# Optimization experiments

Hardware: AMD Instinct MI355X
Metric: run time of the kernel (lower is better)

Reference implementation:

```python
import jax, jax.numpy as jnp
import numpy as np

B, P = 256, 4096
H, W = 512, 512


def setup_inputs() -> dict:
    key = jax.random.key(0)
    k1, k2, k3 = jax.random.split(key, 3)
    indices = jax.random.randint(k1, (B, P, 2), 0, min(H, W), dtype=jnp.int64)
    num_valid = jax.random.randint(k2, (B,), 0, P, dtype=jnp.int32)
    feats = jax.random.normal(k3, (B, P, 1), dtype=jnp.float32)
    return {"indices": indices, "num_valid_coordinates": num_valid, "padded_features": feats}


def reference(indices, num_valid_coordinates, padded_features):
    # mask of valid (non-padded) points per sample: [B, P]
    mask = jnp.arange(P, dtype=num_valid_coordinates.dtype)[None, :] < num_valid_coordinates[:, None]
    vals = jnp.squeeze(padded_features, axis=-1) * mask.astype(padded_features.dtype)  # [B, P]
    # send invalid points out of bounds so JAX drops those scatter writes
    idx = jnp.where(mask[:, :, None], indices, H)  # [B, P, 2]
    b = jnp.broadcast_to(jnp.arange(B)[:, None], (B, P))
    out = jnp.zeros((B, H, W), dtype=padded_features.dtype)
    # single vectorized batched scatter-add (duplicate coordinates sum,
    # matching SparseTensor densification semantics)
    out = out.at[b, idx[..., 0], idx[..., 1]].add(vals)
    return out
```

## Files before the change

kernel.cpp:

```cpp
#include <hip/hip_runtime.h>

#define BATCH 256
#define PTS   4096
#define HH    512
#define WW    512

#define ROWS_PER_TILE 16
#define TILES (HH / ROWS_PER_TILE)
#define TILE_ELEMS (ROWS_PER_TILE * WW)

typedef float f32x4 __attribute__((ext_vector_type(4)));

__global__ __launch_bounds__(256) void tile_gather_kernel(
        const int* __restrict__ indices,
        const int* __restrict__ num_valid,
        const float* __restrict__ feats,
        float* __restrict__ out)
{
    __shared__ float tile[TILE_ELEMS];

    int i = blockIdx.x;
    int xcd  = i & 7;
    int slot = i >> 3;
    int b = xcd * (BATCH / 8) + (slot >> 5);
    int t = slot & (TILES - 1);
    int r0 = t * ROWS_PER_TILE;
    int tidx = threadIdx.x;

    f32x4* tile4 = reinterpret_cast<f32x4*>(tile);
    #pragma unroll
    for (int k = tidx; k < TILE_ELEMS / 4; k += 256)
        tile4[k] = (f32x4){0.f, 0.f, 0.f, 0.f};

    int nv = num_valid[b];
    __syncthreads();

    const int4* idx4 = reinterpret_cast<const int4*>(indices) + (size_t)b * (PTS / 2);
    const float* fb  = feats + (size_t)b * PTS;

    int n4 = (nv + 1) >> 1;
    for (int q = tidx; q < n4; q += 256) {
        int4 two = idx4[q];
        int r0a = two.x - r0;
        if ((unsigned)r0a < ROWS_PER_TILE)
            atomicAdd(&tile[r0a * WW + two.y], fb[2 * q]);
        int p1 = 2 * q + 1;
        int r1a = two.z - r0;
        if (p1 < nv && (unsigned)r1a < ROWS_PER_TILE)
            atomicAdd(&tile[r1a * WW + two.w], fb[p1]);
    }
    __syncthreads();

    float* ob = out + (size_t)b * (HH * WW) + (size_t)r0 * WW;
    f32x4* dst = reinterpret_cast<f32x4*>(ob);
    #pragma unroll
    for (int k = tidx; k < TILE_ELEMS / 4; k += 256)
        __builtin_nontemporal_store(tile4[k], dst + k);
}

extern "C" void kernel_launch(void* const* d_in, const int* in_sizes, int n_in,
                              void* d_out, int out_size, void* d_ws, size_t ws_size,
                              hipStream_t stream) {
    const int*   indices   = (const int*)d_in[0];
    const int*   num_valid = (const int*)d_in[1];
    const float* feats     = (const float*)d_in[2];
    float*       out       = (float*)d_out;

    tile_gather_kernel<<<BATCH * TILES, 256, 0, stream>>>(indices, num_valid, feats, out);
}
```

Measured before the change: 50.88 us.

## Bin points by row tile in a pre-pass before tile scatter

Adds a per-batch binning kernel that counts points per 16-row tile, prefix-sums the counts, and writes compacted (offset, value) entries into workspace. The tile kernel then reads only its own bin instead of scanning every point of the sample for each of the 32 tiles. This removes the redundant 32x reading of indices, at the cost of an extra kernel launch, a workspace round trip, and a serial prefix sum in one thread per batch.

```diff
diff --git a/kernel.cpp b/kernel.cpp
--- a/kernel.cpp
+++ b/kernel.cpp
@@ -11,10 +11,59 @@
 
 typedef float f32x4 __attribute__((ext_vector_type(4)));
 
-__global__ __launch_bounds__(256) void tile_gather_kernel(
+#define ENTRIES_BYTES ((size_t)BATCH * PTS * 8)
+
+__global__ __launch_bounds__(1024) void bin_kernel(
         const int* __restrict__ indices,
         const int* __restrict__ num_valid,
         const float* __restrict__ feats,
+        uint2* __restrict__ entries,
+        unsigned* __restrict__ counts,
+        unsigned* __restrict__ offsets)
+{
+    __shared__ unsigned cnt[TILES];
+    __shared__ unsigned cur[TILES];
+
+    int b = blockIdx.x;
+    int tidx = threadIdx.x;
+    if (tidx < TILES) cnt[tidx] = 0;
+    int nv = num_valid[b];
+    __syncthreads();
+
+    const int2* idx2 = reinterpret_cast<const int2*>(indices) + (size_t)b * PTS;
+
+    for (int p = tidx; p < nv; p += 1024)
+        atomicAdd(&cnt[((unsigned)idx2[p].x) >> 4], 1u);
+    __syncthreads();
+
+    if (tidx == 0) {
+        unsigned run = 0;
+        for (int i = 0; i < TILES; ++i) { cur[i] = run; run += cnt[i]; }
+    }
+    __syncthreads();
+
+    if (tidx < TILES) {
+        counts[b * TILES + tidx]  = cnt[tidx];
+        offsets[b * TILES + tidx] = cur[tidx];
+    }
+    __syncthreads();
+
+    const float* fb = feats + (size_t)b * PTS;
+    uint2* eb = entries + (size_t)b * PTS;
+    for (int p = tidx; p < nv; p += 1024) {
+        int2 ij = idx2[p];
+        float v = fb[p];
+        unsigned bin = ((unsigned)ij.x) >> 4;
+        unsigned pos = atomicAdd(&cur[bin], 1u);
+        eb[pos] = make_uint2((unsigned)((ij.x & (ROWS_PER_TILE - 1)) * WW + ij.y),
+                             __float_as_uint(v));
+    }
+}
+
+__global__ __launch_bounds__(256) void tile_write_kernel(
+        const uint2* __restrict__ entries,
+        const unsigned* __restrict__ counts,
+        const unsigned* __restrict__ offsets,
         float* __restrict__ out)
 {
     __shared__ float tile[TILE_ELEMS];
@@ -24,7 +73,6 @@
     int slot = i >> 3;
     int b = xcd * (BATCH / 8) + (slot >> 5);
     int t = slot & (TILES - 1);
-    int r0 = t * ROWS_PER_TILE;
     int tidx = threadIdx.x;
 
     f32x4* tile4 = reinterpret_cast<f32x4*>(tile);
@@ -32,26 +80,18 @@
     for (int k = tidx; k < TILE_ELEMS / 4; k += 256)
         tile4[k] = (f32x4){0.f, 0.f, 0.f, 0.f};
 
-    int nv = num_valid[b];
+    unsigned n   = counts[b * TILES + t];
+    unsigned off = offsets[b * TILES + t];
     __syncthreads();
 
-    const int4* idx4 = reinterpret_cast<const int4*>(indices) + (size_t)b * (PTS / 2);
-    const float* fb  = feats + (size_t)b * PTS;
-
-    int n4 = (nv + 1) >> 1;
-    for (int q = tidx; q < n4; q += 256) {
-        int4 two = idx4[q];
-        int r0a = two.x - r0;
-        if ((unsigned)r0a < ROWS_PER_TILE)
-            atomicAdd(&tile[r0a * WW + two.y], fb[2 * q]);
-        int p1 = 2 * q + 1;
-        int r1a = two.z - r0;
-        if (p1 < nv && (unsigned)r1a < ROWS_PER_TILE)
-            atomicAdd(&tile[r1a * WW + two.w], fb[p1]);
+    const uint2* eb = entries + (size_t)b * PTS + off;
+    for (unsigned e = tidx; e < n; e += 256) {
+        uint2 ent = eb[e];
+        atomicAdd(&tile[ent.x], __uint_as_float(ent.y));
     }
     __syncthreads();
 
-    float* ob = out + (size_t)b * (HH * WW) + (size_t)r0 * WW;
+    float* ob = out + (size_t)b * (HH * WW) + (size_t)t * TILE_ELEMS;
     f32x4* dst = reinterpret_cast<f32x4*>(ob);
     #pragma unroll
     for (int k = tidx; k < TILE_ELEMS / 4; k += 256)
@@ -66,5 +106,12 @@
     const float* feats     = (const float*)d_in[2];
     float*       out       = (float*)d_out;
 
-    tile_gather_kernel<<<BATCH * TILES, 256, 0, stream>>>(indices, num_valid, feats, out);
+    uint2*    entries = (uint2*)d_ws;
+    unsigned* counts  = (unsigned*)((char*)d_ws + ENTRIES_BYTES);
+    unsigned* offsets = counts + BATCH * TILES;
+
+    bin_kernel<<<BATCH, 1024, 0, stream>>>(indices, num_valid, feats,
+                                           entries, counts, offsets);
+    tile_write_kernel<<<BATCH * TILES, 256, 0, stream>>>(entries, counts,
+                                                         offsets, out);
 }
```

After: 56.23 us. 10.5% more time.
